# Optimization experiments

Hardware: AMD Instinct MI355X
Metric: run time of the kernel (lower is better)

## Reference

```python
import jax, jax.numpy as jnp
import numpy as np

B, L, C, H, W = 2, 16, 16, 64, 64


def setup_inputs() -> dict:
    key = jax.random.key(0)
    k1, k2 = jax.random.split(key)
    # flows scaled so cumulative normalized-coordinate flows mostly stay in [-1, 1]
    flows = jax.random.normal(k1, (B, L, 2, H, W), dtype=jnp.float32) * 0.05
    images = jax.random.normal(k2, (B, L, C, H, W), dtype=jnp.float32)
    return {"flows": flows, "images": images}


def _bilinear_sample(images, gx, gy):
    # images: [B, Lj, C, H, W]; gx, gy: [B, Li, Lj, H, W] normalized coords in [-1, 1]
    # Replicates torch.nn.functional.grid_sample(mode='bilinear',
    # padding_mode='zeros', align_corners=False).
    Bs, Lj, Cs, Hs, Ws = images.shape
    ix = ((gx + 1.0) * Ws - 1.0) * 0.5  # pixel x coord
    iy = ((gy + 1.0) * Hs - 1.0) * 0.5  # pixel y coord
    x0f = jnp.floor(ix)
    y0f = jnp.floor(iy)
    wx = ix - x0f  # weight toward x0+1 (differentiable w.r.t. flow)
    wy = iy - y0f
    x0 = x0f.astype(jnp.int32)
    y0 = y0f.astype(jnp.int32)
    img_flat = images.reshape(Bs, Lj, Cs, Hs * Ws)

    def gather(xi, yi):
        valid = (xi >= 0) & (xi < Ws) & (yi >= 0) & (yi < Hs)  # [B,Li,Lj,H,W]
        lin = jnp.clip(yi, 0, Hs - 1) * Ws + jnp.clip(xi, 0, Ws - 1)
        lin_t = jnp.transpose(lin, (0, 2, 1, 3, 4))  # [B,Lj,Li,H,W]
        # per (b, j): gather [C, HW] at indices [Li, H, W] -> [C, Li, H, W]
        v = jax.vmap(jax.vmap(lambda im, l: im[:, l]))(img_flat, lin_t)
        v = jnp.transpose(v, (0, 3, 1, 2, 4, 5))  # [B,Li,Lj,C,H,W]
        return v * valid[:, :, :, None, :, :].astype(v.dtype)

    v00 = gather(x0, y0)
    v01 = gather(x0 + 1, y0)
    v10 = gather(x0, y0 + 1)
    v11 = gather(x0 + 1, y0 + 1)
    wX = wx[:, :, :, None, :, :]
    wY = wy[:, :, :, None, :, :]
    return (v00 * (1.0 - wX) * (1.0 - wY) + v01 * wX * (1.0 - wY)
            + v10 * (1.0 - wX) * wY + v11 * wX * wY)


def reference(flows, images):
    Bs, Ls, _, Hs, Ws = flows.shape
    dt = flows.dtype
    cum = jnp.cumsum(flows, axis=1)  # [B,L,2,H,W]
    # rel[b, i, j] = cum[b, i] - cum[b, j]  -> [B,Li,Lj,2,H,W]
    rel = cum[:, :, None] - cum[:, None, :]
    # base sampling grid (pixel centers in normalized coords)
    gx_base = (jnp.arange(Ws, dtype=dt) + 0.5) * (2.0 / Ws) - 1.0  # [W]
    gy_base = (jnp.arange(Hs, dtype=dt) + 0.5) * (2.0 / Hs) - 1.0  # [H]
    gx = gx_base + rel[:, :, :, 0]              # [B,Li,Lj,H,W]
    gy = gy_base[:, None] + rel[:, :, :, 1]     # [B,Li,Lj,H,W]
    gx = jnp.remainder(gx + 1.0, 2.0) - 1.0     # wrap x into [-1, 1)
    warped = _bilinear_sample(images, gx, gy)   # [B,Li,Lj,C,H,W]
    mask = jnp.tril(jnp.ones((Ls, Ls), dtype=dt))
    # causal accumulate over source index j
    return jnp.einsum('bijchw,ij->bichw', warped, mask)
```

## Files before the change

kernel.cpp:

```cpp
#include <hip/hip_runtime.h>

#define BB 2
#define LL 16
#define CC 16
#define HH 64
#define WW 64
#define HWSZ (HH * WW)
#define NSEG 36

__device__ __constant__ int SEG_I[NSEG] = {
    1, 2, 3, 4,
    5, 5, 6, 6, 7, 7, 8, 8,
    9, 9, 9, 10, 10, 10, 11, 11, 11, 12, 12, 12,
    13, 13, 13, 13, 14, 14, 14, 14, 15, 15, 15, 15};
__device__ __constant__ int SEG_J0[NSEG] = {
    0, 0, 0, 0,
    0, 4, 0, 4, 0, 4, 0, 4,
    0, 4, 8, 0, 4, 8, 0, 4, 8, 0, 4, 8,
    0, 4, 8, 12, 0, 4, 8, 12, 0, 4, 8, 12};

__global__ __launch_bounds__(256) void gsp_cumsum(
    const float* __restrict__ flows,
    float* __restrict__ cum)
{
    const int gid = blockIdx.x * 256 + threadIdx.x;
    const int b    = gid / (2 * HWSZ);
    const int r    = gid % (2 * HWSZ);
    const int comp = r / HWSZ;
    const int pix  = r % HWSZ;

    float v[LL];
    #pragma unroll
    for (int l = 0; l < LL; ++l)
        v[l] = flows[((size_t)(b * LL + l) * 2 + comp) * HWSZ + pix];
    #pragma unroll
    for (int l = 1; l < LL; ++l) v[l] += v[l - 1];
    #pragma unroll
    for (int l = 0; l < LL; ++l)
        cum[((size_t)(b * LL + l) * 2 + comp) * HWSZ + pix] = v[l];
}

__global__ __launch_bounds__(256) void gsp_transpose(
    const float* __restrict__ images, float4* __restrict__ nhwc)
{
    const int gid  = blockIdx.x * 256 + threadIdx.x;
    const int quad = gid & 3;
    const int pix  = (gid >> 2) & (HWSZ - 1);
    const int bl   = gid >> 14;

    const float* src = images + (size_t)(bl * CC + quad * 4) * HWSZ + pix;
    float4 v;
    v.x = src[0 * HWSZ];
    v.y = src[1 * HWSZ];
    v.z = src[2 * HWSZ];
    v.w = src[3 * HWSZ];
    nhwc[(size_t)(bl * HWSZ + pix) * 4 + quad] = v;
}

__global__ __launch_bounds__(256) void gsp_identity(
    const float4* __restrict__ images, float4* __restrict__ out)
{
    const int idx = blockIdx.x * 256 + threadIdx.x;
    out[idx] = images[idx];
}

__global__ __launch_bounds__(256) void gsp_pairs(
    const float* __restrict__ cum,
    const float* __restrict__ nhwc,
    float* __restrict__ out)
{
    const int tile = blockIdx.x & 63;
    const int seg  = (blockIdx.x >> 6) % NSEG;
    const int b    = blockIdx.x / (64 * NSEG);

    const int i    = SEG_I[seg];
    const int j0   = SEG_J0[seg];
    const int jmax = i - 1;

    const int psub = threadIdx.x >> 2;
    const int quad = threadIdx.x & 3;
    const int pix  = tile * 64 + psub;
    const int h = pix >> 6;
    const int w = pix & (WW - 1);

    const float* cum_b  = cum + (size_t)b * LL * 2 * HWSZ;
    const float* nhwc_b = nhwc + (size_t)b * LL * HWSZ * CC;

    const float gxb = (w + 0.5f) * (2.0f / WW) - 1.0f;
    const float gyb = (h + 0.5f) * (2.0f / HH) - 1.0f;

    const float cix = cum_b[(size_t)i * 2 * HWSZ + pix];
    const float ciy = cum_b[(size_t)i * 2 * HWSZ + HWSZ + pix];

    float ax = 0.0f, ay = 0.0f, az = 0.0f, aw = 0.0f;

    #pragma unroll
    for (int k = 0; k < 4; ++k) {
        const int jraw = j0 + k;
        const int j = min(jraw, jmax);
        const float wpad = (jraw <= jmax) ? 1.0f : 0.0f;

        const float cjx = cum_b[(size_t)j * 2 * HWSZ + pix];
        const float cjy = cum_b[(size_t)j * 2 * HWSZ + HWSZ + pix];

        float gx = gxb + (cix - cjx);
        float gy = gyb + (ciy - cjy);

        float tt = gx + 1.0f;
        tt = tt - floorf(tt * 0.5f) * 2.0f;
        gx = tt - 1.0f;

        const float ix = ((gx + 1.0f) * WW - 1.0f) * 0.5f;
        const float iy = ((gy + 1.0f) * HH - 1.0f) * 0.5f;
        const float x0f = floorf(ix);
        const float y0f = floorf(iy);
        const float fx = ix - x0f;
        const float fy = iy - y0f;
        const int x0 = (int)x0f;
        const int y0 = (int)y0f;
        const int x1 = x0 + 1;
        const int y1 = y0 + 1;

        const bool vx0 = (x0 >= 0) && (x0 < WW);
        const bool vx1 = (x1 >= 0) && (x1 < WW);
        const bool vy0 = (y0 >= 0) && (y0 < HH);
        const bool vy1 = (y1 >= 0) && (y1 < HH);

        const int cx0 = min(max(x0, 0), WW - 1);
        const int cx1 = min(max(x1, 0), WW - 1);
        const int cy0 = min(max(y0, 0), HH - 1);
        const int cy1 = min(max(y1, 0), HH - 1);

        const float w00 = wpad * (1.0f - fx) * (1.0f - fy) * ((vx0 && vy0) ? 1.0f : 0.0f);
        const float w01 = wpad * fx * (1.0f - fy)          * ((vx1 && vy0) ? 1.0f : 0.0f);
        const float w10 = wpad * (1.0f - fx) * fy          * ((vx0 && vy1) ? 1.0f : 0.0f);
        const float w11 = wpad * fx * fy                   * ((vx1 && vy1) ? 1.0f : 0.0f);

        const int o00 = cy0 * WW + cx0;
        const int o01 = cy0 * WW + cx1;
        const int o10 = cy1 * WW + cx0;
        const int o11 = cy1 * WW + cx1;

        const float4* jb = (const float4*)(nhwc_b + (size_t)j * HWSZ * CC);
        const float4 v00 = jb[o00 * 4 + quad];
        const float4 v01 = jb[o01 * 4 + quad];
        const float4 v10 = jb[o10 * 4 + quad];
        const float4 v11 = jb[o11 * 4 + quad];

        ax += w00 * v00.x + w01 * v01.x + w10 * v10.x + w11 * v11.x;
        ay += w00 * v00.y + w01 * v01.y + w10 * v10.y + w11 * v11.y;
        az += w00 * v00.z + w01 * v01.z + w10 * v10.z + w11 * v11.z;
        aw += w00 * v00.w + w01 * v01.w + w10 * v10.w + w11 * v11.w;
    }

    float* op = out + ((size_t)(b * LL + i) * CC + quad * 4) * HWSZ + pix;
    atomicAdd(op + 0 * HWSZ, ax);
    atomicAdd(op + 1 * HWSZ, ay);
    atomicAdd(op + 2 * HWSZ, az);
    atomicAdd(op + 3 * HWSZ, aw);
}

extern "C" void kernel_launch(void* const* d_in, const int* in_sizes, int n_in,
                              void* d_out, int out_size, void* d_ws, size_t ws_size,
                              hipStream_t stream) {
    const float* flows  = (const float*)d_in[0];
    const float* images = (const float*)d_in[1];
    float* out = (float*)d_out;
    float* cum  = (float*)d_ws;
    float* nhwc = (float*)d_ws + (BB * LL * 2 * HWSZ);

    gsp_cumsum<<<BB * 2 * HWSZ / 256, 256, 0, stream>>>(flows, cum);

    gsp_transpose<<<BB * LL * HWSZ * 4 / 256, 256, 0, stream>>>(images, (float4*)nhwc);

    const int n4 = BB * LL * CC * HWSZ / 4;
    gsp_identity<<<n4 / 256, 256, 0, stream>>>((const float4*)images, (float4*)out);

    const int grid = BB * NSEG * 64;
    gsp_pairs<<<grid, 256, 0, stream>>>(cum, nhwc, out);
}
```

Before: 94.27 us.

## Fuse cumsum, transpose and identity copy into one prep kernel; interleave cum as float2

Merges the three preprocessing kernels into a single launch. The first 32 blocks compute the cumulative flow sum and the remaining blocks transpose images to NHWC while also writing the identity term into out from the same loaded values, so images are no longer read twice. Cumulative flows are now stored interleaved as float2, so the pairs kernel fetches x and y together in one load. This removes two launches and one full read of images. The cost is a branch-divergent mixed kernel and an identity write that is no longer vectorized.

```diff
diff --git a/kernel.cpp b/kernel.cpp
--- a/kernel.cpp
+++ b/kernel.cpp
@@ -19,53 +19,58 @@
     0, 4, 8, 0, 4, 8, 0, 4, 8, 0, 4, 8,
     0, 4, 8, 12, 0, 4, 8, 12, 0, 4, 8, 12};
 
-__global__ __launch_bounds__(256) void gsp_cumsum(
+#define CUM2_FLOATS (BB * LL * HWSZ * 2)
+
+__global__ __launch_bounds__(256) void gsp_prep(
     const float* __restrict__ flows,
-    float* __restrict__ cum)
+    const float* __restrict__ images,
+    float2* __restrict__ cum2,
+    float4* __restrict__ nhwc,
+    float* __restrict__ out)
 {
-    const int gid = blockIdx.x * 256 + threadIdx.x;
-    const int b    = gid / (2 * HWSZ);
-    const int r    = gid % (2 * HWSZ);
-    const int comp = r / HWSZ;
-    const int pix  = r % HWSZ;
+    if (blockIdx.x < 32) {
+        const int gid = blockIdx.x * 256 + threadIdx.x;
+        const int b   = gid >> 12;
+        const int pix = gid & (HWSZ - 1);
+        const float* fb = flows + (size_t)b * LL * 2 * HWSZ + pix;
+        float vx[LL], vy[LL];
+        #pragma unroll
+        for (int l = 0; l < LL; ++l) {
+            vx[l] = fb[(size_t)l * 2 * HWSZ];
+            vy[l] = fb[(size_t)l * 2 * HWSZ + HWSZ];
+        }
+        #pragma unroll
+        for (int l = 1; l < LL; ++l) { vx[l] += vx[l - 1]; vy[l] += vy[l - 1]; }
+        float2* cb = cum2 + (size_t)b * LL * HWSZ + pix;
+        #pragma unroll
+        for (int l = 0; l < LL; ++l) {
+            float2 v; v.x = vx[l]; v.y = vy[l];
+            cb[(size_t)l * HWSZ] = v;
+        }
+    } else {
+        const int gid  = (blockIdx.x - 32) * 256 + threadIdx.x;
+        const int quad = gid & 3;
+        const int pix  = (gid >> 2) & (HWSZ - 1);
+        const int bl   = gid >> 14;
 
-    float v[LL];
-    #pragma unroll
-    for (int l = 0; l < LL; ++l)
-        v[l] = flows[((size_t)(b * LL + l) * 2 + comp) * HWSZ + pix];
-    #pragma unroll
-    for (int l = 1; l < LL; ++l) v[l] += v[l - 1];
-    #pragma unroll
-    for (int l = 0; l < LL; ++l)
-        cum[((size_t)(b * LL + l) * 2 + comp) * HWSZ + pix] = v[l];
-}
+        const float* src = images + (size_t)(bl * CC + quad * 4) * HWSZ + pix;
+        float4 v;
+        v.x = src[0 * HWSZ];
+        v.y = src[1 * HWSZ];
+        v.z = src[2 * HWSZ];
+        v.w = src[3 * HWSZ];
+        nhwc[(size_t)(bl * HWSZ + pix) * 4 + quad] = v;
 
-__global__ __launch_bounds__(256) void gsp_transpose(
-    const float* __restrict__ images, float4* __restrict__ nhwc)
-{
-    const int gid  = blockIdx.x * 256 + threadIdx.x;
-    const int quad = gid & 3;
-    const int pix  = (gid >> 2) & (HWSZ - 1);
-    const int bl   = gid >> 14;
-
-    const float* src = images + (size_t)(bl * CC + quad * 4) * HWSZ + pix;
-    float4 v;
-    v.x = src[0 * HWSZ];
-    v.y = src[1 * HWSZ];
-    v.z = src[2 * HWSZ];
-    v.w = src[3 * HWSZ];
-    nhwc[(size_t)(bl * HWSZ + pix) * 4 + quad] = v;
-}
-
-__global__ __launch_bounds__(256) void gsp_identity(
-    const float4* __restrict__ images, float4* __restrict__ out)
-{
-    const int idx = blockIdx.x * 256 + threadIdx.x;
-    out[idx] = images[idx];
+        float* op = out + (size_t)(bl * CC + quad * 4) * HWSZ + pix;
+        op[0 * HWSZ] = v.x;
+        op[1 * HWSZ] = v.y;
+        op[2 * HWSZ] = v.z;
+        op[3 * HWSZ] = v.w;
+    }
 }
 
 __global__ __launch_bounds__(256) void gsp_pairs(
-    const float* __restrict__ cum,
+    const float2* __restrict__ cum2,
     const float* __restrict__ nhwc,
     float* __restrict__ out)
 {
@@ -83,14 +88,13 @@
     const int h = pix >> 6;
     const int w = pix & (WW - 1);
 
-    const float* cum_b  = cum + (size_t)b * LL * 2 * HWSZ;
+    const float2* cum_b = cum2 + (size_t)b * LL * HWSZ + pix;
     const float* nhwc_b = nhwc + (size_t)b * LL * HWSZ * CC;
 
     const float gxb = (w + 0.5f) * (2.0f / WW) - 1.0f;
     const float gyb = (h + 0.5f) * (2.0f / HH) - 1.0f;
 
-    const float cix = cum_b[(size_t)i * 2 * HWSZ + pix];
-    const float ciy = cum_b[(size_t)i * 2 * HWSZ + HWSZ + pix];
+    const float2 ci = cum_b[(size_t)i * HWSZ];
 
     float ax = 0.0f, ay = 0.0f, az = 0.0f, aw = 0.0f;
 
@@ -100,11 +104,10 @@
         const int j = min(jraw, jmax);
         const float wpad = (jraw <= jmax) ? 1.0f : 0.0f;
 
-        const float cjx = cum_b[(size_t)j * 2 * HWSZ + pix];
-        const float cjy = cum_b[(size_t)j * 2 * HWSZ + HWSZ + pix];
+        const float2 cj = cum_b[(size_t)j * HWSZ];
 
-        float gx = gxb + (cix - cjx);
-        float gy = gyb + (ciy - cjy);
+        float gx = gxb + (ci.x - cj.x);
+        float gy = gyb + (ci.y - cj.y);
 
         float tt = gx + 1.0f;
         tt = tt - floorf(tt * 0.5f) * 2.0f;
@@ -166,16 +169,11 @@
     const float* flows  = (const float*)d_in[0];
     const float* images = (const float*)d_in[1];
     float* out = (float*)d_out;
-    float* cum  = (float*)d_ws;
-    float* nhwc = (float*)d_ws + (BB * LL * 2 * HWSZ);
+    float2* cum2 = (float2*)d_ws;
+    float*  nhwc = (float*)d_ws + CUM2_FLOATS;
 
-    gsp_cumsum<<<BB * 2 * HWSZ / 256, 256, 0, stream>>>(flows, cum);
-
-    gsp_transpose<<<BB * LL * HWSZ * 4 / 256, 256, 0, stream>>>(images, (float4*)nhwc);
-
-    const int n4 = BB * LL * CC * HWSZ / 4;
-    gsp_identity<<<n4 / 256, 256, 0, stream>>>((const float4*)images, (float4*)out);
+    gsp_prep<<<32 + 2048, 256, 0, stream>>>(flows, images, cum2, (float4*)nhwc, out);
 
     const int grid = BB * NSEG * 64;
-    gsp_pairs<<<grid, 256, 0, stream>>>(cum, nhwc, out);
+    gsp_pairs<<<grid, 256, 0, stream>>>(cum2, nhwc, out);
 }
```

Result: faster. 91.84 us (-2.6%).
